# Performance work log

Hardware: AMD Instinct MI355X
Metric: run time of the kernel (lower is better)

The kernel has to match this reference:

```python
import jax, jax.numpy as jnp
import numpy as np

D = 1024      # hidden_dim
E = 8         # num_experts
H = 4096      # expert_hidden_dim (= 4*D, module default)
K = 2         # top-k experts per token


def setup_inputs() -> dict:
    key = jax.random.key(0)
    ks = jax.random.split(key, 7)
    s = 1.0 / np.sqrt(D)
    sh = 1.0 / np.sqrt(H)
    return {
        "x": jax.random.normal(ks[0], (4, 1024, D), dtype=jnp.float32),
        "W1": jax.random.uniform(ks[1], (E, D, H), jnp.float32, -s, s),
        "b1": jax.random.uniform(ks[2], (E, H), jnp.float32, -s, s),
        "W2": jax.random.uniform(ks[3], (E, H, D), jnp.float32, -sh, sh),
        "b2": jax.random.uniform(ks[4], (E, D), jnp.float32, -sh, sh),
        "Wg": jax.random.uniform(ks[5], (D, E), jnp.float32, -s, s),
        "bg": jax.random.uniform(ks[6], (E,), jnp.float32, -s, s),
    }


def reference(x, W1, b1, W2, b2, Wg, bg):
    orig_shape = x.shape
    x2d = x.reshape(-1, D)                                    # [N, D]
    gate_scores = jax.nn.softmax(x2d @ Wg + bg, axis=-1)      # [N, E]
    topk_scores, topk_idx = jax.lax.top_k(gate_scores, K)     # [N, K]
    # Dense all-experts 2-layer MLP (dropout is identity in eval mode)
    h = jax.nn.gelu(jnp.einsum('nd,edh->neh', x2d, W1) + b1[None], approximate=False)  # [N, E, H]
    expert_out = jnp.einsum('neh,ehd->ned', h, W2) + b2[None]  # [N, E, D]
    # Gather top-k expert outputs and combine with gate weights
    topk_out = jnp.take_along_axis(expert_out, topk_idx[:, :, None], axis=1)  # [N, K, D]
    out = jnp.sum(topk_out * topk_scores[:, :, None], axis=1)  # [N, D]
    return out.reshape(orig_shape)
```

## Files before the change

kernel.cpp:

```cpp
#include <hip/hip_runtime.h>
#include <math.h>

#define DIM  1024
#define NEXP 8
#define HID  4096
#define TOPK 2

typedef __attribute__((ext_vector_type(8))) short bf16x8;
typedef __attribute__((ext_vector_type(4))) float f32x4;

__device__ inline unsigned short f2bf(float f) {
  union { float f; unsigned int u; } v; v.f = f;
  unsigned int u = v.u;
  return (unsigned short)((u + 0x7FFFu + ((u >> 16) & 1u)) >> 16);
}

__device__ inline void load_lds16(const void* g, void* l) {
  __builtin_amdgcn_global_load_lds(
      (const __attribute__((address_space(1))) void*)g,
      (__attribute__((address_space(3))) void*)l, 16, 0, 0);
}

__global__ void gate_kernel(const float* __restrict__ x,
                            const float* __restrict__ Wg,
                            const float* __restrict__ bg,
                            float* __restrict__ topk_score,
                            int* __restrict__ count,
                            int* __restrict__ lists,
                            int N) {
  int n = blockIdx.x;
  if (n >= N) return;
  int lane = threadIdx.x;
  float acc[NEXP];
#pragma unroll
  for (int e = 0; e < NEXP; ++e) acc[e] = 0.f;
  const float* xr = x + (size_t)n * DIM;
  for (int d = lane; d < DIM; d += 64) {
    float xv = xr[d];
    const float* w = Wg + (size_t)d * NEXP;
#pragma unroll
    for (int e = 0; e < NEXP; ++e) acc[e] += xv * w[e];
  }
#pragma unroll
  for (int off = 32; off > 0; off >>= 1) {
#pragma unroll
    for (int e = 0; e < NEXP; ++e) acc[e] += __shfl_xor(acc[e], off, 64);
  }
  if (lane == 0) {
    float l[NEXP];
#pragma unroll
    for (int e = 0; e < NEXP; ++e) l[e] = acc[e] + bg[e];
    float m = l[0];
#pragma unroll
    for (int e = 1; e < NEXP; ++e) m = fmaxf(m, l[e]);
    float p[NEXP];
    float s = 0.f;
#pragma unroll
    for (int e = 0; e < NEXP; ++e) { p[e] = expf(l[e] - m); s += p[e]; }
    int i0 = 0;
#pragma unroll
    for (int e = 1; e < NEXP; ++e) if (l[e] > l[i0]) i0 = e;
    int i1 = (i0 == 0) ? 1 : 0;
#pragma unroll
    for (int e = 0; e < NEXP; ++e) if (e != i0 && l[e] > l[i1]) i1 = e;
    float inv = 1.f / s;
    topk_score[n * TOPK + 0] = p[i0] * inv;
    topk_score[n * TOPK + 1] = p[i1] * inv;
    int pos0 = atomicAdd(&count[i0], 1);
    lists[(size_t)i0 * N + pos0] = n * TOPK + 0;
    int pos1 = atomicAdd(&count[i1], 1);
    lists[(size_t)i1 * N + pos1] = n * TOPK + 1;
  }
}

__global__ void offsets_kernel(const int* __restrict__ count, int* __restrict__ offsets,
                               int* __restrict__ tiles, int* __restrict__ ntiles) {
  if (threadIdx.x == 0 && blockIdx.x == 0) {
    int s = 0, nt = 0;
    for (int e = 0; e < NEXP; ++e) {
      offsets[e] = s;
      int c = count[e];
      s += c;
      int rts = (c + 127) >> 7;
      for (int i = 0; i < rts; ++i) tiles[nt++] = (e << 16) | i;
    }
    offsets[NEXP] = s;
    ntiles[0] = nt;
  }
}

__global__ void gather_kernel(const float* __restrict__ x,
                              const int* __restrict__ offsets,
                              const int* __restrict__ lists,
                              unsigned short* __restrict__ Xg,
                              int* __restrict__ pairmap,
                              int N) {
  int g = blockIdx.x;
  int e = 0;
  while (e < NEXP - 1 && g >= offsets[e + 1]) ++e;
  int i = g - offsets[e];
  int ent = lists[(size_t)e * N + i];
  int tok = ent >> 1;
  if (threadIdx.x == 0) pairmap[g] = ent;
  float4 v = *((const float4*)(x + (size_t)tok * DIM) + threadIdx.x);
  ushort4 o;
  o.x = f2bf(v.x); o.y = f2bf(v.y); o.z = f2bf(v.z); o.w = f2bf(v.w);
  *((ushort4*)(Xg + (size_t)g * DIM) + threadIdx.x) = o;
}

__global__ __launch_bounds__(256) void transpose_convert(
    const float* __restrict__ src, unsigned short* __restrict__ dst, int R, int C) {
  const int e = blockIdx.z;
  src += (size_t)e * R * C;
  dst += (size_t)e * R * C;
  const int r0 = blockIdx.x * 64, c0 = blockIdx.y * 64;
  __shared__ unsigned short Ts[64][68];
  const int t = threadIdx.x;
  const int rr = t >> 4, cc = (t & 15) * 4;
#pragma unroll
  for (int p = 0; p < 4; ++p) {
    int r = rr + p * 16;
    float4 v = *(const float4*)(src + (size_t)(r0 + r) * C + c0 + cc);
    Ts[cc + 0][r] = f2bf(v.x);
    Ts[cc + 1][r] = f2bf(v.y);
    Ts[cc + 2][r] = f2bf(v.z);
    Ts[cc + 3][r] = f2bf(v.w);
  }
  __syncthreads();
  const int cr = t >> 3, rq = (t & 7) * 8;
#pragma unroll
  for (int p = 0; p < 2; ++p) {
    int c = cr + p * 32;
    ushort4 a = *(ushort4*)&Ts[c][rq];
    ushort4 b = *(ushort4*)&Ts[c][rq + 4];
    *(ushort4*)(dst + (size_t)(c0 + c) * R + r0 + rq) = a;
    *(ushort4*)(dst + (size_t)(c0 + c) * R + r0 + rq + 4) = b;
  }
}

template <int PASS>
__global__ __launch_bounds__(256, 2) void moe_gemm6(
    const unsigned short* __restrict__ Asrc,
    const unsigned short* __restrict__ Bt,
    const float* __restrict__ bias,
    const int* __restrict__ offsets,
    const int* __restrict__ tiles,
    const int* __restrict__ ntiles,
    const int* __restrict__ pairmap,
    const float* __restrict__ score,
    unsigned short* __restrict__ Hmat,
    float* __restrict__ out,
    int maxt) {
  constexpr int K  = (PASS == 1) ? DIM : HID;
  constexpr int NS = (PASS == 1) ? HID : DIM;
  constexpr int KS = (PASS == 1) ? 1 : 2;
  constexpr int KL = K / KS;
  constexpr int NT = KL / 64;

  const unsigned orig = blockIdx.x;
  const unsigned nwg = gridDim.x;
  const unsigned q = nwg >> 3, r8 = nwg & 7;
  const unsigned xcd = orig & 7, p8 = orig >> 3;
  const unsigned id = (xcd < r8 ? xcd * (q + 1) : r8 * (q + 1) + (xcd - r8) * q) + p8;
  const int tt = (int)(id % (unsigned)maxt);
  const int ct = (int)(id / (unsigned)maxt);

  if (tt >= ntiles[0]) return;
  const int pk = tiles[tt];
  const int e  = pk >> 16;
  const int rt = pk & 0xffff;
  const int gbase = offsets[e];
  const int nc = offsets[e + 1] - gbase;
  const int rowsvalid = min(128, nc - rt * 128);
  const int kz = (PASS == 1) ? 0 : blockIdx.z;
  const int koff = kz * KL;

  __shared__ unsigned short As[2][8192];
  __shared__ unsigned short Bs[2][8192];

  const int tid  = threadIdx.x;
  const int lane = tid & 63;
  const int w    = tid >> 6;
  const int wr = (w >> 1) * 64;
  const int wc = (w & 1) * 64;
  const int fr = lane & 15;
  const int fq = lane >> 4;

  f32x4 acc[4][4];
#pragma unroll
  for (int m = 0; m < 4; ++m)
#pragma unroll
    for (int n = 0; n < 4; ++n) acc[m][n] = (f32x4){0.f, 0.f, 0.f, 0.f};

  const unsigned short* Ab = Asrc + (size_t)(gbase + rt * 128) * K + koff;
  const unsigned short* Bb = Bt + (size_t)e * NS * K + (size_t)ct * 128 * K + koff;

  const int srow  = tid >> 3;
  const int sunit = tid & 7;
  const int sswz  = sunit ^ (srow & 7);

  auto stage = [&](int b, int k0) {
#pragma unroll
    for (int is = 0; is < 4; ++is) {
      const int row = is * 32 + srow;
      load_lds16(Ab + (size_t)row * K + k0 + sswz * 8, (char*)As[b] + is * 4096 + tid * 16);
      load_lds16(Bb + (size_t)row * K + k0 + sswz * 8, (char*)Bs[b] + is * 4096 + tid * 16);
    }
  };

  stage(0, 0);

  for (int t = 0; t < NT; ++t) {
    if (t + 1 < NT) {
      stage((t + 1) & 1, (t + 1) * 64);
      asm volatile("s_waitcnt vmcnt(8)" ::: "memory");
    } else {
      asm volatile("s_waitcnt vmcnt(0)" ::: "memory");
    }
    __builtin_amdgcn_s_barrier();

    const unsigned short* Ac = As[t & 1];
    const unsigned short* Bc = Bs[t & 1];
    bf16x8 af[2][4], bfv[2][4];
#pragma unroll
    for (int kk = 0; kk < 2; ++kk) {
      const int au = ((kk * 4 + fq) ^ (fr & 7)) * 8;
#pragma unroll
      for (int m = 0; m < 4; ++m)
        af[kk][m] = *(const bf16x8*)&Ac[(wr + m * 16 + fr) * 64 + au];
#pragma unroll
      for (int n = 0; n < 4; ++n)
        bfv[kk][n] = *(const bf16x8*)&Bc[(wc + n * 16 + fr) * 64 + au];
    }
    __builtin_amdgcn_s_setprio(1);
#pragma unroll
    for (int kk = 0; kk < 2; ++kk)
#pragma unroll
      for (int m = 0; m < 4; ++m)
#pragma unroll
        for (int n = 0; n < 4; ++n)
          acc[m][n] = __builtin_amdgcn_mfma_f32_16x16x32_bf16(af[kk][m], bfv[kk][n], acc[m][n], 0, 0, 0);
    __builtin_amdgcn_s_setprio(0);
    __builtin_amdgcn_s_barrier();
  }

  if (PASS == 1) {
#pragma unroll
    for (int n = 0; n < 4; ++n) {
      const int col = ct * 128 + wc + n * 16 + fr;
      const float b1v = bias[(size_t)e * NS + col];
#pragma unroll
      for (int m = 0; m < 4; ++m) {
#pragma unroll
        for (int r = 0; r < 4; ++r) {
          const int lrow = wr + m * 16 + fq * 4 + r;
          if (lrow < rowsvalid) {
            float v = acc[m][n][r] + b1v;
            v = 0.5f * v * (1.f + erff(v * 0.70710678118654752440f));
            Hmat[(size_t)(gbase + rt * 128 + lrow) * HID + col] = f2bf(v);
          }
        }
      }
    }
  } else {
    float b2v[4];
#pragma unroll
    for (int n = 0; n < 4; ++n)
      b2v[n] = (kz == 0) ? bias[(size_t)e * NS + ct * 128 + wc + n * 16 + fr] : 0.f;
#pragma unroll
    for (int m = 0; m < 4; ++m) {
#pragma unroll
      for (int r = 0; r < 4; ++r) {
        const int lrow = wr + m * 16 + fq * 4 + r;
        if (lrow < rowsvalid) {
          const int g = gbase + rt * 128 + lrow;
          const int ent = pairmap[g];
          const int tok = ent >> 1;
          const float s = score[ent];
#pragma unroll
          for (int n = 0; n < 4; ++n) {
            const int col = ct * 128 + wc + n * 16 + fr;
            atomicAdd(&out[(size_t)tok * DIM + col], s * (acc[m][n][r] + b2v[n]));
          }
        }
      }
    }
  }
}

template <int PASS>
__global__ __launch_bounds__(256) void moe_gemm(
    const unsigned short* __restrict__ Asrc,
    const float* __restrict__ Bsrc,
    const float* __restrict__ bias,
    const int* __restrict__ offsets,
    const int* __restrict__ pairmap,
    const float* __restrict__ score,
    unsigned short* __restrict__ Hmat,
    float* __restrict__ out) {
  constexpr int K  = (PASS == 1) ? DIM : HID;
  constexpr int NS = (PASS == 1) ? HID : DIM;
  const int e = blockIdx.z;
  const int gbase = offsets[e];
  const int nc = offsets[e + 1] - gbase;
  const int rt = blockIdx.x;
  if (rt * 128 >= nc) return;
  const int rowsvalid = min(128, nc - rt * 128);
  const int ct = blockIdx.y;
  __shared__ unsigned short As[128 * 40];
  __shared__ unsigned short Bs[128 * 40];
  const int tid  = threadIdx.x;
  const int lane = tid & 63;
  const int wid  = tid >> 6;
  const int wr = (wid >> 1) * 64;
  const int wc = (wid & 1) * 64;
  const int fr = lane & 15;
  const int fq = lane >> 4;
  f32x4 acc[4][4];
#pragma unroll
  for (int m = 0; m < 4; ++m)
#pragma unroll
    for (int n = 0; n < 4; ++n) acc[m][n] = (f32x4){0.f, 0.f, 0.f, 0.f};
  const int ar = tid >> 1;
  const int ak = (tid & 1) * 16;
  int arow = rt * 128 + ((ar < rowsvalid) ? ar : 0);
  const unsigned short* Aptr = Asrc + (size_t)(gbase + arow) * K + ak;
  const int bc = (tid & 31) * 4;
  const int bk = (tid >> 5) * 4;
  const float* Bptr = Bsrc + (size_t)e * K * NS + (size_t)bk * NS + ct * 128 + bc;
  for (int k0 = 0; k0 < K; k0 += 32) {
    uint4 av0 = *(const uint4*)(Aptr + k0);
    uint4 av1 = *(const uint4*)(Aptr + k0 + 8);
    const float* bp = Bptr + (size_t)k0 * NS;
    float4 w0 = *(const float4*)(bp);
    float4 w1 = *(const float4*)(bp + NS);
    float4 w2 = *(const float4*)(bp + 2 * NS);
    float4 w3 = *(const float4*)(bp + 3 * NS);
    __syncthreads();
    *(uint4*)&As[ar * 40 + ak]     = av0;
    *(uint4*)&As[ar * 40 + ak + 8] = av1;
    {
      uint2 pv;
      pv.x = (unsigned int)f2bf(w0.x) | ((unsigned int)f2bf(w1.x) << 16);
      pv.y = (unsigned int)f2bf(w2.x) | ((unsigned int)f2bf(w3.x) << 16);
      *(uint2*)&Bs[(bc + 0) * 40 + bk] = pv;
      pv.x = (unsigned int)f2bf(w0.y) | ((unsigned int)f2bf(w1.y) << 16);
      pv.y = (unsigned int)f2bf(w2.y) | ((unsigned int)f2bf(w3.y) << 16);
      *(uint2*)&Bs[(bc + 1) * 40 + bk] = pv;
      pv.x = (unsigned int)f2bf(w0.z) | ((unsigned int)f2bf(w1.z) << 16);
      pv.y = (unsigned int)f2bf(w2.z) | ((unsigned int)f2bf(w3.z) << 16);
      *(uint2*)&Bs[(bc + 2) * 40 + bk] = pv;
      pv.x = (unsigned int)f2bf(w0.w) | ((unsigned int)f2bf(w1.w) << 16);
      pv.y = (unsigned int)f2bf(w2.w) | ((unsigned int)f2bf(w3.w) << 16);
      *(uint2*)&Bs[(bc + 3) * 40 + bk] = pv;
    }
    __syncthreads();
    bf16x8 af[4], bfr[4];
#pragma unroll
    for (int m = 0; m < 4; ++m)
      af[m] = *(const bf16x8*)&As[(wr + m * 16 + fr) * 40 + fq * 8];
#pragma unroll
    for (int n = 0; n < 4; ++n)
      bfr[n] = *(const bf16x8*)&Bs[(wc + n * 16 + fr) * 40 + fq * 8];
#pragma unroll
    for (int m = 0; m < 4; ++m)
#pragma unroll
      for (int n = 0; n < 4; ++n)
        acc[m][n] = __builtin_amdgcn_mfma_f32_16x16x32_bf16(af[m], bfr[n], acc[m][n], 0, 0, 0);
  }
  if (PASS == 1) {
#pragma unroll
    for (int n = 0; n < 4; ++n) {
      int col = ct * 128 + wc + n * 16 + fr;
      float b1v = bias[(size_t)e * NS + col];
#pragma unroll
      for (int m = 0; m < 4; ++m) {
#pragma unroll
        for (int r = 0; r < 4; ++r) {
          int lrow = wr + m * 16 + fq * 4 + r;
          if (lrow < rowsvalid) {
            float v = acc[m][n][r] + b1v;
            v = 0.5f * v * (1.f + erff(v * 0.70710678118654752440f));
            Hmat[(size_t)(gbase + rt * 128 + lrow) * HID + col] = f2bf(v);
          }
        }
      }
    }
  } else {
    float b2v[4];
#pragma unroll
    for (int n = 0; n < 4; ++n)
      b2v[n] = bias[(size_t)e * NS + ct * 128 + wc + n * 16 + fr];
#pragma unroll
    for (int m = 0; m < 4; ++m) {
#pragma unroll
      for (int r = 0; r < 4; ++r) {
        int lrow = wr + m * 16 + fq * 4 + r;
        if (lrow < rowsvalid) {
          int g = gbase + rt * 128 + lrow;
          int ent = pairmap[g];
          int tok = ent >> 1;
          float s = score[ent];
#pragma unroll
          for (int n = 0; n < 4; ++n) {
            int col = ct * 128 + wc + n * 16 + fr;
            atomicAdd(&out[(size_t)tok * DIM + col], s * (acc[m][n][r] + b2v[n]));
          }
        }
      }
    }
  }
}

extern "C" void kernel_launch(void* const* d_in, const int* in_sizes, int n_in,
                              void* d_out, int out_size, void* d_ws, size_t ws_size,
                              hipStream_t stream) {
  const float* x  = (const float*)d_in[0];
  const float* W1 = (const float*)d_in[1];
  const float* b1 = (const float*)d_in[2];
  const float* W2 = (const float*)d_in[3];
  const float* b2 = (const float*)d_in[4];
  const float* Wg = (const float*)d_in[5];
  const float* bg = (const float*)d_in[6];
  float* out = (float*)d_out;
  const int N  = in_sizes[0] / DIM;
  const int NP = N * TOPK;
  const int MAXT = NP / 128 + NEXP;

  char* ws = (char*)d_ws;
  size_t off = 0;
  auto alloc = [&](size_t bytes) -> void* {
    void* p = ws + off;
    off = (off + bytes + 255) & ~(size_t)255;
    return p;
  };
  int*   count      = (int*)alloc(NEXP * sizeof(int));
  int*   offsets    = (int*)alloc((NEXP + 1) * sizeof(int));
  int*   tiles      = (int*)alloc((size_t)MAXT * sizeof(int));
  int*   ntiles     = (int*)alloc(sizeof(int));
  float* topk_score = (float*)alloc((size_t)NP * sizeof(float));
  int*   lists      = (int*)alloc((size_t)NEXP * N * sizeof(int));
  int*   pairmap    = (int*)alloc((size_t)NP * sizeof(int));
  unsigned short* Xg   = (unsigned short*)alloc((size_t)(NP + 256) * DIM * sizeof(unsigned short));
  unsigned short* Hmat = (unsigned short*)alloc((size_t)(NP + 256) * HID * sizeof(unsigned short));
  unsigned short* W1T = (unsigned short*)alloc((size_t)NEXP * DIM * HID * sizeof(unsigned short));
  unsigned short* W2T = (unsigned short*)alloc((size_t)NEXP * HID * DIM * sizeof(unsigned short));
  size_t need_full = off;

  hipMemsetAsync(count, 0, NEXP * sizeof(int), stream);
  gate_kernel<<<N, 64, 0, stream>>>(x, Wg, bg, topk_score, count, lists, N);
  offsets_kernel<<<1, 64, 0, stream>>>(count, offsets, tiles, ntiles);
  gather_kernel<<<NP, DIM / 4, 0, stream>>>(x, offsets, lists, Xg, pairmap, N);
  hipMemsetAsync(out, 0, (size_t)out_size * sizeof(float), stream);

  if (ws_size >= need_full) {
    dim3 tg1(DIM / 64, HID / 64, NEXP);
    transpose_convert<<<tg1, 256, 0, stream>>>(W1, W1T, DIM, HID);
    dim3 tg2(HID / 64, DIM / 64, NEXP);
    transpose_convert<<<tg2, 256, 0, stream>>>(W2, W2T, HID, DIM);

    dim3 g1((HID / 128) * MAXT, 1, 1);
    moe_gemm6<1><<<g1, 256, 0, stream>>>(Xg, W1T, b1, offsets, tiles, ntiles,
                                         pairmap, topk_score, Hmat, out, MAXT);
    dim3 g2((DIM / 128) * MAXT, 1, 2);
    moe_gemm6<2><<<g2, 256, 0, stream>>>(Hmat, W2T, b2, offsets, tiles, ntiles,
                                         pairmap, topk_score, Hmat, out, MAXT);
  } else {
    const int RT = (N + 127) / 128;
    dim3 g1(RT, HID / 128, NEXP);
    moe_gemm<1><<<g1, 256, 0, stream>>>(Xg, W1, b1, offsets, pairmap, topk_score, Hmat, out);
    dim3 g2(RT, DIM / 128, NEXP);
    moe_gemm<2><<<g2, 256, 0, stream>>>(Hmat, W2, b2, offsets, pairmap, topk_score, Hmat, out);
  }
}
```

Measured before the change: 558.8 us.

## Enlarge grouped MoE GEMM tiles to 256x256 with 512-thread blocks

Both expert GEMM passes now use 256x256 output tiles per workgroup instead of 128x128. Each block has 8 waves arranged 2x4, and each wave computes a 128x64 sub-tile. Row tiling in the offsets kernel, the LDS staging, the swizzled fragment loads and the epilogue indexing are all changed to match. The goal is twice the data reuse per byte of global and LDS traffic. In exchange, each block holds about 128 KB of double-buffered LDS and more accumulator registers, there are fewer blocks to fill the CUs (notably in the split-K second pass), and padding waste grows on each expert's last partial row tile.

```diff
diff --git a/kernel.cpp b/kernel.cpp
--- a/kernel.cpp
+++ b/kernel.cpp
@@ -81,7 +81,7 @@
       offsets[e] = s;
       int c = count[e];
       s += c;
-      int rts = (c + 127) >> 7;
+      int rts = (c + 255) >> 8;
       for (int i = 0; i < rts; ++i) tiles[nt++] = (e << 16) | i;
     }
     offsets[NEXP] = s;
@@ -139,7 +139,7 @@
 }
 
 template <int PASS>
-__global__ __launch_bounds__(256, 2) void moe_gemm6(
+__global__ __launch_bounds__(512, 2) void moe_gemm7(
     const unsigned short* __restrict__ Asrc,
     const unsigned short* __restrict__ Bt,
     const float* __restrict__ bias,
@@ -171,40 +171,38 @@
   const int rt = pk & 0xffff;
   const int gbase = offsets[e];
   const int nc = offsets[e + 1] - gbase;
-  const int rowsvalid = min(128, nc - rt * 128);
+  const int rowsvalid = min(256, nc - rt * 256);
   const int kz = (PASS == 1) ? 0 : blockIdx.z;
   const int koff = kz * KL;
 
-  __shared__ unsigned short As[2][8192];
-  __shared__ unsigned short Bs[2][8192];
+  __shared__ unsigned short As[2][16384];
+  __shared__ unsigned short Bs[2][16384];
 
   const int tid  = threadIdx.x;
   const int lane = tid & 63;
-  const int w    = tid >> 6;
-  const int wr = (w >> 1) * 64;
-  const int wc = (w & 1) * 64;
+  const int wid  = tid >> 6;
+  const int wr = (wid >> 2) * 128;
+  const int wc = (wid & 3) * 64;
   const int fr = lane & 15;
   const int fq = lane >> 4;
 
-  f32x4 acc[4][4];
-#pragma unroll
-  for (int m = 0; m < 4; ++m)
+  f32x4 acc[8][4];
+#pragma unroll
+  for (int m = 0; m < 8; ++m)
 #pragma unroll
     for (int n = 0; n < 4; ++n) acc[m][n] = (f32x4){0.f, 0.f, 0.f, 0.f};
 
-  const unsigned short* Ab = Asrc + (size_t)(gbase + rt * 128) * K + koff;
-  const unsigned short* Bb = Bt + (size_t)e * NS * K + (size_t)ct * 128 * K + koff;
-
-  const int srow  = tid >> 3;
-  const int sunit = tid & 7;
-  const int sswz  = sunit ^ (srow & 7);
+  const unsigned short* Ab = Asrc + (size_t)(gbase + rt * 256) * K + koff;
+  const unsigned short* Bb = Bt + (size_t)e * NS * K + (size_t)ct * 256 * K + koff;
 
   auto stage = [&](int b, int k0) {
 #pragma unroll
-    for (int is = 0; is < 4; ++is) {
-      const int row = is * 32 + srow;
-      load_lds16(Ab + (size_t)row * K + k0 + sswz * 8, (char*)As[b] + is * 4096 + tid * 16);
-      load_lds16(Bb + (size_t)row * K + k0 + sswz * 8, (char*)Bs[b] + is * 4096 + tid * 16);
+    for (int i = 0; i < 4; ++i) {
+      const int c = i * 512 + tid;
+      const int row = c >> 3;
+      const int swz = (c & 7) ^ (row & 7);
+      load_lds16(Ab + (size_t)row * K + k0 + swz * 8, (char*)As[b] + c * 16);
+      load_lds16(Bb + (size_t)row * K + k0 + swz * 8, (char*)Bs[b] + c * 16);
     }
   };
 
@@ -221,43 +219,46 @@
 
     const unsigned short* Ac = As[t & 1];
     const unsigned short* Bc = Bs[t & 1];
-    bf16x8 af[2][4], bfv[2][4];
 #pragma unroll
     for (int kk = 0; kk < 2; ++kk) {
-      const int au = ((kk * 4 + fq) ^ (fr & 7)) * 8;
-#pragma unroll
-      for (int m = 0; m < 4; ++m)
-        af[kk][m] = *(const bf16x8*)&Ac[(wr + m * 16 + fr) * 64 + au];
-#pragma unroll
-      for (int n = 0; n < 4; ++n)
-        bfv[kk][n] = *(const bf16x8*)&Bc[(wc + n * 16 + fr) * 64 + au];
-    }
-    __builtin_amdgcn_s_setprio(1);
-#pragma unroll
-    for (int kk = 0; kk < 2; ++kk)
-#pragma unroll
-      for (int m = 0; m < 4; ++m)
+      bf16x8 af[8], bf[4];
+#pragma unroll
+      for (int m = 0; m < 8; ++m) {
+        const int row = wr + m * 16 + fr;
+        const int u = (kk * 4 + fq) ^ (row & 7);
+        af[m] = *(const bf16x8*)&Ac[row * 64 + u * 8];
+      }
+#pragma unroll
+      for (int n = 0; n < 4; ++n) {
+        const int row = wc + n * 16 + fr;
+        const int u = (kk * 4 + fq) ^ (row & 7);
+        bf[n] = *(const bf16x8*)&Bc[row * 64 + u * 8];
+      }
+      __builtin_amdgcn_s_setprio(1);
+#pragma unroll
+      for (int m = 0; m < 8; ++m)
 #pragma unroll
         for (int n = 0; n < 4; ++n)
-          acc[m][n] = __builtin_amdgcn_mfma_f32_16x16x32_bf16(af[kk][m], bfv[kk][n], acc[m][n], 0, 0, 0);
-    __builtin_amdgcn_s_setprio(0);
+          acc[m][n] = __builtin_amdgcn_mfma_f32_16x16x32_bf16(af[m], bf[n], acc[m][n], 0, 0, 0);
+      __builtin_amdgcn_s_setprio(0);
+    }
     __builtin_amdgcn_s_barrier();
   }
 
   if (PASS == 1) {
 #pragma unroll
     for (int n = 0; n < 4; ++n) {
-      const int col = ct * 128 + wc + n * 16 + fr;
+      const int col = ct * 256 + wc + n * 16 + fr;
       const float b1v = bias[(size_t)e * NS + col];
 #pragma unroll
-      for (int m = 0; m < 4; ++m) {
+      for (int m = 0; m < 8; ++m) {
 #pragma unroll
         for (int r = 0; r < 4; ++r) {
           const int lrow = wr + m * 16 + fq * 4 + r;
           if (lrow < rowsvalid) {
             float v = acc[m][n][r] + b1v;
             v = 0.5f * v * (1.f + erff(v * 0.70710678118654752440f));
-            Hmat[(size_t)(gbase + rt * 128 + lrow) * HID + col] = f2bf(v);
+            Hmat[(size_t)(gbase + rt * 256 + lrow) * HID + col] = f2bf(v);
           }
         }
       }
@@ -266,20 +267,20 @@
     float b2v[4];
 #pragma unroll
     for (int n = 0; n < 4; ++n)
-      b2v[n] = (kz == 0) ? bias[(size_t)e * NS + ct * 128 + wc + n * 16 + fr] : 0.f;
-#pragma unroll
-    for (int m = 0; m < 4; ++m) {
+      b2v[n] = (kz == 0) ? bias[(size_t)e * NS + ct * 256 + wc + n * 16 + fr] : 0.f;
+#pragma unroll
+    for (int m = 0; m < 8; ++m) {
 #pragma unroll
       for (int r = 0; r < 4; ++r) {
         const int lrow = wr + m * 16 + fq * 4 + r;
         if (lrow < rowsvalid) {
-          const int g = gbase + rt * 128 + lrow;
+          const int g = gbase + rt * 256 + lrow;
           const int ent = pairmap[g];
           const int tok = ent >> 1;
           const float s = score[ent];
 #pragma unroll
           for (int n = 0; n < 4; ++n) {
-            const int col = ct * 128 + wc + n * 16 + fr;
+            const int col = ct * 256 + wc + n * 16 + fr;
             atomicAdd(&out[(size_t)tok * DIM + col], s * (acc[m][n][r] + b2v[n]));
           }
         }
@@ -425,7 +426,7 @@
   float* out = (float*)d_out;
   const int N  = in_sizes[0] / DIM;
   const int NP = N * TOPK;
-  const int MAXT = NP / 128 + NEXP;
+  const int MAXT = NP / 256 + NEXP;
 
   char* ws = (char*)d_ws;
   size_t off = 0;
@@ -459,11 +460,11 @@
     dim3 tg2(HID / 64, DIM / 64, NEXP);
     transpose_convert<<<tg2, 256, 0, stream>>>(W2, W2T, HID, DIM);
 
-    dim3 g1((HID / 128) * MAXT, 1, 1);
-    moe_gemm6<1><<<g1, 256, 0, stream>>>(Xg, W1T, b1, offsets, tiles, ntiles,
+    dim3 g1((HID / 256) * MAXT, 1, 1);
+    moe_gemm7<1><<<g1, 512, 0, stream>>>(Xg, W1T, b1, offsets, tiles, ntiles,
                                          pairmap, topk_score, Hmat, out, MAXT);
-    dim3 g2((DIM / 128) * MAXT, 1, 2);
-    moe_gemm6<2><<<g2, 256, 0, stream>>>(Hmat, W2T, b2, offsets, tiles, ntiles,
+    dim3 g2((DIM / 256) * MAXT, 1, 2);
+    moe_gemm7<2><<<g2, 512, 0, stream>>>(Hmat, W2T, b2, offsets, tiles, ntiles,
                                          pairmap, topk_score, Hmat, out, MAXT);
   } else {
     const int RT = (N + 127) / 128;
```

New measurement: 598.9 us. 7.2% more time.
